# Kernel optimization log

Measured on AMD Instinct MI355X. Metric: run time of the kernel, lower is better.

## Reference

```python
import jax, jax.numpy as jnp
import numpy as np

B, S, D = 2, 2048, 1024
H = 16
HD = D // H


def setup_inputs() -> dict:
    key = jax.random.key(0)
    ks = jax.random.split(key, 6)
    x = jax.random.normal(ks[0], (B, S, D), dtype=jnp.float32)
    scale = 1.0 / np.sqrt(D)
    Wq = jax.random.normal(ks[1], (D, D), dtype=jnp.float32) * scale
    Wk = jax.random.normal(ks[2], (D, D), dtype=jnp.float32) * scale
    Wv = jax.random.normal(ks[3], (D, D), dtype=jnp.float32) * scale
    Wo = jax.random.normal(ks[4], (D, D), dtype=jnp.float32) * scale
    bo = jax.random.normal(ks[5], (D,), dtype=jnp.float32) * 0.01
    return {"x": x, "Wq": Wq, "Wk": Wk, "Wv": Wv, "Wo": Wo, "bo": bo}


def reference(x, Wq, Wk, Wv, Wo, bo):
    b, t, _ = x.shape
    # QKV projections (no bias), split into heads: [b, h, t, hd]
    q = (x @ Wq).reshape(b, t, H, HD).transpose(0, 2, 1, 3)
    k = (x @ Wk).reshape(b, t, H, HD).transpose(0, 2, 1, 3)
    v = (x @ Wv).reshape(b, t, H, HD).transpose(0, 2, 1, 3)
    # scores [b, h, t, t]; causal mask (upper triangle -> -inf) applied before scaling
    scores = jnp.einsum("bhqd,bhkd->bhqk", q, k)
    causal = jnp.triu(jnp.ones((t, t), dtype=bool), k=1)
    scores = jnp.where(causal, -jnp.inf, scores)
    attn = jax.nn.softmax(scores / jnp.sqrt(jnp.asarray(HD, scores.dtype)), axis=-1)
    ctx = jnp.einsum("bhqk,bhkd->bhqd", attn, v)
    ctx = ctx.transpose(0, 2, 1, 3).reshape(b, t, H * HD)
    return ctx @ Wo + bo
```

## Files before the change

### kernel.cpp

```cpp
#include <hip/hip_runtime.h>

#define B_ 2
#define S_ 2048
#define D_ 1024
#define H_ 16
#define HD_ 64
#define M_ (B_*S_)

typedef __attribute__((ext_vector_type(8))) short bf16x8;
typedef __attribute__((ext_vector_type(4))) short s16x4;
typedef __attribute__((ext_vector_type(4))) float f32x4;
typedef __attribute__((ext_vector_type(4))) unsigned int u32x4;

static __device__ __forceinline__ unsigned short f2bf(float f) {
  unsigned int u = __builtin_bit_cast(unsigned int, f);
  u += 0x7FFFu + ((u >> 16) & 1u);
  return (unsigned short)(u >> 16);
}

static __device__ __forceinline__ unsigned int cvt_pk_bf16(float a, float b) {
  unsigned int r;
  asm("v_cvt_pk_bf16_f32 %0, %1, %2" : "=v"(r) : "v"(a), "v"(b));
  return r;
}

static __device__ __forceinline__ void gload_lds16(const void* g, void* l) {
  __builtin_amdgcn_global_load_lds(
      (const __attribute__((address_space(1))) unsigned int*)g,
      (__attribute__((address_space(3))) unsigned int*)l, 16, 0, 0);
}

__global__ __launch_bounds__(256) void xcvt_kernel(const float* __restrict__ x,
                                                   unsigned short* __restrict__ xb) {
  size_t i = ((size_t)blockIdx.x * 256 + threadIdx.x) * 8;
  float4 a = ((const float4*)(x + i))[0];
  float4 b = ((const float4*)(x + i))[1];
  bf16x8 w;
  w[0]=(short)f2bf(a.x); w[1]=(short)f2bf(a.y); w[2]=(short)f2bf(a.z); w[3]=(short)f2bf(a.w);
  w[4]=(short)f2bf(b.x); w[5]=(short)f2bf(b.y); w[6]=(short)f2bf(b.z); w[7]=(short)f2bf(b.w);
  *(bf16x8*)(xb + i) = w;
}

__global__ void wtrans_kernel(const float* __restrict__ Wq, const float* __restrict__ Wk,
                              const float* __restrict__ Wv, const float* __restrict__ Wo,
                              unsigned short* __restrict__ wt) {
  __shared__ float tile[32][33];
  const float* W = blockIdx.z==0 ? Wq : blockIdx.z==1 ? Wk : blockIdx.z==2 ? Wv : Wo;
  unsigned short* out = wt + (size_t)blockIdx.z * D_ * D_;
  int n0 = blockIdx.x*32, k0 = blockIdx.y*32;
  int tx = threadIdx.x, ty = threadIdx.y;
  #pragma unroll
  for (int i=0;i<4;i++) tile[ty+i*8][tx] = W[(size_t)(k0+ty+i*8)*D_ + n0+tx];
  __syncthreads();
  #pragma unroll
  for (int i=0;i<4;i++) out[(size_t)(n0+ty+i*8)*D_ + (k0+tx)] = f2bf(tile[tx][ty+i*8]);
}

#define GEMM_K_LOOP(Abase, Bbase)                                                     \
  for (int ks = 0; ks < 16; ++ks) {                                                   \
    const int k0 = ks * 64;                                                           \
    __syncthreads();                                                                  \
    _Pragma("unroll")                                                                 \
    for (int p = 0; p < 4; ++p) {                                                     \
      int c = p*256 + t;                                                              \
      int row = c >> 3, sl = (c & 7) ^ (row & 7);                                     \
      gload_lds16(Abase + (size_t)row*D_ + k0 + sl*8, &As[(p*256 + wid*64)*8]);       \
    }                                                                                 \
    _Pragma("unroll")                                                                 \
    for (int p = 0; p < 4; ++p) {                                                     \
      int c = p*256 + t;                                                              \
      int row = c >> 3, sl = (c & 7) ^ (row & 7);                                     \
      gload_lds16(Bbase + (size_t)row*D_ + k0 + sl*8, &Bs[(p*256 + wid*64)*8]);       \
    }                                                                                 \
    __syncthreads();                                                                  \
    _Pragma("unroll")                                                                 \
    for (int kk = 0; kk < 2; ++kk) {                                                  \
      bf16x8 af[4], bfr[4];                                                           \
      _Pragma("unroll")                                                               \
      for (int m = 0; m < 4; ++m) {                                                   \
        int row = wr + m*16 + l15;                                                    \
        af[m] = *(const bf16x8*)((const char*)As + row*128 + (((kk*4+lg)^(row&7))<<4)); \
      }                                                                               \
      _Pragma("unroll")                                                               \
      for (int n = 0; n < 4; ++n) {                                                   \
        int row = wc + n*16 + l15;                                                    \
        bfr[n] = *(const bf16x8*)((const char*)Bs + row*128 + (((kk*4+lg)^(row&7))<<4)); \
      }                                                                               \
      _Pragma("unroll")                                                               \
      for (int m = 0; m < 4; ++m)                                                     \
        _Pragma("unroll")                                                             \
        for (int n = 0; n < 4; ++n)                                                   \
          acc[m][n] = __builtin_amdgcn_mfma_f32_16x16x32_bf16(af[m], bfr[n], acc[m][n], 0,0,0); \
    }                                                                                 \
  }

__global__ __launch_bounds__(256,3) void gemm_qkv_kernel(
    const unsigned short* __restrict__ xb, const unsigned short* __restrict__ wt,
    unsigned short* __restrict__ Qo, unsigned short* __restrict__ Ko,
    unsigned short* __restrict__ Vto) {
  __shared__ __align__(16) unsigned short As[128*64];
  __shared__ __align__(16) unsigned short Bs[128*64];
  const int z = blockIdx.z;
  const int m0 = blockIdx.y*128, n0 = blockIdx.x*128;
  const int t = threadIdx.x, lane = t & 63, wid = t >> 6;
  const int wr = (wid>>1)*64, wc = (wid&1)*64;
  const int l15 = lane & 15, lg = lane >> 4;
  const unsigned short* Ab = xb + (size_t)m0 * D_;
  const unsigned short* Bb = wt + (size_t)z * D_ * D_ + (size_t)n0 * D_;

  f32x4 acc[4][4];
  #pragma unroll
  for (int m=0;m<4;m++)
    #pragma unroll
    for (int n=0;n<4;n++) acc[m][n] = f32x4{0.f,0.f,0.f,0.f};

  GEMM_K_LOOP(Ab, Bb)

  const float qscale = 0.18033688011112042f;
  #pragma unroll
  for (int m=0;m<4;m++) {
    #pragma unroll
    for (int n=0;n<4;n++) {
      #pragma unroll
      for (int r=0;r<4;r++) {
        int gm = m0 + wr + m*16 + lg*4 + r;
        int gn = n0 + wc + n*16 + l15;
        int b = gm >> 11, s = gm & (S_-1);
        int h = gn >> 6,  d = gn & 63;
        float av = acc[m][n][r];
        if (z==0) av *= qscale;
        unsigned short val = f2bf(av);
        if (z==0)      Qo[(((size_t)(b*H_+h))*S_ + s)*HD_ + d] = val;
        else if (z==1) Ko[(((size_t)(b*H_+h))*S_ + s)*HD_ + d] = val;
        else           Vto[(((size_t)(b*H_+h))*HD_ + d)*S_ + s] = val;
      }
    }
  }
}

__global__ __launch_bounds__(256,3) void attn_kernel(
    const unsigned short* __restrict__ Q, const unsigned short* __restrict__ K,
    const unsigned short* __restrict__ Vt, unsigned short* __restrict__ ctx) {
  __shared__ __align__(16) unsigned short KT[2][64*64];
  __shared__ __align__(16) unsigned short VT[2][64*64];
  __shared__ float LS[2][64];
  const int t = threadIdx.x, lane = t & 63, wid = t >> 6;
  const int bh = blockIdx.x & 31;
  const int qt = 31 - (int)(blockIdx.x >> 5);
  const int b = bh >> 4, h = bh & 15;
  const int q0 = qt * 64;
  const int nchunk = qt + 1;
  const unsigned short* Qp = Q  + (size_t)bh * S_ * HD_;
  const unsigned short* Kp = K  + (size_t)bh * S_ * HD_;
  const unsigned short* Vp = Vt + (size_t)bh * HD_ * S_;
  const int l15 = lane & 15, lg = lane >> 4;
  const int rsub = lane >> 3, slot = lane & 7;
  const int sslot = slot ^ rsub;

  bf16x8 qf0[4], qf1[4];
  #pragma unroll
  for (int j=0;j<4;j++) {
    qf0[j] = *(const bf16x8*)(Qp + (size_t)(q0 + j*16 + l15)*HD_ + lg*8);
    qf1[j] = *(const bf16x8*)(Qp + (size_t)(q0 + j*16 + l15)*HD_ + 32 + lg*8);
  }

  f32x4 o[4][4];
  f32x4 accl[4];
  #pragma unroll
  for (int j=0;j<4;j++) {
    accl[j] = f32x4{0.f,0.f,0.f,0.f};
    #pragma unroll
    for (int dt=0;dt<4;dt++) o[j][dt] = f32x4{0.f,0.f,0.f,0.f};
  }
  s16x4 ones;
  ones[0] = (short)0x3F80; ones[1] = (short)0x3F80;
  ones[2] = (short)0x3F80; ones[3] = (short)0x3F80;

  const unsigned short* kS0 = Kp + (size_t)(16*wid + rsub)*HD_ + sslot*8;
  const unsigned short* kS1 = kS0 + 8*HD_;
  const unsigned short* vS0 = Vp + (size_t)(16*wid + rsub)*S_ + sslot*8;
  const unsigned short* vS1 = vS0 + 8*S_;

  auto stage = [&](int buf) {
    unsigned short* kd = &KT[buf][16*wid*64];
    unsigned short* vd = &VT[buf][16*wid*64];
    gload_lds16(kS0, kd);
    gload_lds16(kS1, kd + 8*64);
    gload_lds16(vS0, vd);
    gload_lds16(vS1, vd + 8*64);
    kS0 += 64*HD_; kS1 += 64*HD_;
    vS0 += 64;     vS1 += 64;
  };

  const int krow = wid*16 + l15;
  const int ksw = (krow & 7) << 4;

  auto body = [&](int cur, bool domask) {
    const char* Kt = (const char*)&KT[cur][0];
    const char* Vv = (const char*)&VT[cur][0];

    bf16x8 kf0 = *(const bf16x8*)(Kt + krow*128 + ((lg*16)      ^ ksw));
    bf16x8 kf1 = *(const bf16x8*)(Kt + krow*128 + ((64 + lg*16) ^ ksw));
    s16x4 vb[4];
    #pragma unroll
    for (int dt=0;dt<4;dt++) {
      int vrow = dt*16 + l15;
      int vsw = (vrow & 7) << 4;
      vb[dt] = *(const s16x4*)(Vv + vrow*128 + ((wid*32 + lg*8) ^ vsw));
    }

    f32x4 st[4];
    __builtin_amdgcn_s_setprio(1);
    #pragma unroll
    for (int j=0;j<4;j++) {
      f32x4 z = f32x4{0.f,0.f,0.f,0.f};
      z = __builtin_amdgcn_mfma_f32_16x16x32_bf16(kf0, qf0[j], z, 0,0,0);
      z = __builtin_amdgcn_mfma_f32_16x16x32_bf16(kf1, qf1[j], z, 0,0,0);
      st[j] = z;
    }
    __builtin_amdgcn_s_setprio(0);

    if (domask) {
      #pragma unroll
      for (int j=0;j<4;j++)
        #pragma unroll
        for (int r=0;r<4;r++)
          if (wid*16 + lg*4 + r > j*16 + l15) st[j][r] = -INFINITY;
    }

    s16x4 pa[4];
    #pragma unroll
    for (int j=0;j<4;j++) {
      float p0 = exp2f(st[j][0]);
      float p1 = exp2f(st[j][1]);
      float p2 = exp2f(st[j][2]);
      float p3 = exp2f(st[j][3]);
      uint2 u;
      u.x = cvt_pk_bf16(p0, p1);
      u.y = cvt_pk_bf16(p2, p3);
      pa[j] = __builtin_bit_cast(s16x4, u);
    }

    __builtin_amdgcn_s_setprio(1);
    #pragma unroll
    for (int j=0;j<4;j++)
      accl[j] = __builtin_amdgcn_mfma_f32_16x16x16bf16_1k(pa[j], ones, accl[j], 0,0,0);
    #pragma unroll
    for (int j=0;j<4;j++)
      #pragma unroll
      for (int dt=0;dt<4;dt++)
        o[j][dt] = __builtin_amdgcn_mfma_f32_16x16x16bf16_1k(pa[j], vb[dt], o[j][dt], 0,0,0);
    __builtin_amdgcn_s_setprio(0);
  };

  stage(0);
  __syncthreads();

  int cur = 0;
  for (int ch=0; ch<nchunk-1; ++ch) {
    stage(cur^1);
    body(cur, false);
    __syncthreads();
    cur ^= 1;
  }
  body(cur, true);

  float* bufA = (float*)&KT[0][0];
  float* bufB = (float*)&VT[0][0];
  __syncthreads();

  if (wid & 1) {
    float* dst = (wid == 1) ? bufA : bufB;
    #pragma unroll
    for (int j=0;j<4;j++) {
      #pragma unroll
      for (int dt=0;dt<4;dt++)
        #pragma unroll
        for (int r=0;r<4;r++)
          dst[(j*16 + lg*4 + r)*64 + dt*16 + l15] = o[j][dt][r];
      if (l15 == 0)
        #pragma unroll
        for (int r=0;r<4;r++) LS[wid>>1][j*16 + lg*4 + r] = accl[j][r];
    }
  }
  __syncthreads();
  if (!(wid & 1)) {
    float* src = (wid == 0) ? bufA : bufB;
    #pragma unroll
    for (int j=0;j<4;j++) {
      #pragma unroll
      for (int dt=0;dt<4;dt++)
        #pragma unroll
        for (int r=0;r<4;r++)
          o[j][dt][r] += src[(j*16 + lg*4 + r)*64 + dt*16 + l15];
      #pragma unroll
      for (int r=0;r<4;r++) accl[j][r] += LS[wid>>1][j*16 + lg*4 + r];
    }
  }
  __syncthreads();
  if (wid == 2) {
    #pragma unroll
    for (int j=0;j<4;j++) {
      #pragma unroll
      for (int dt=0;dt<4;dt++)
        #pragma unroll
        for (int r=0;r<4;r++)
          bufA[(j*16 + lg*4 + r)*64 + dt*16 + l15] = o[j][dt][r];
      if (l15 == 0)
        #pragma unroll
        for (int r=0;r<4;r++) LS[0][j*16 + lg*4 + r] = accl[j][r];
    }
  }
  __syncthreads();
  if (wid == 0) {
    #pragma unroll
    for (int j=0;j<4;j++) {
      #pragma unroll
      for (int dt=0;dt<4;dt++)
        #pragma unroll
        for (int r=0;r<4;r++)
          o[j][dt][r] += bufA[(j*16 + lg*4 + r)*64 + dt*16 + l15];
      #pragma unroll
      for (int r=0;r<4;r++) accl[j][r] += LS[0][j*16 + lg*4 + r];
      float lr[4];
      #pragma unroll
      for (int r=0;r<4;r++) lr[r] = 1.f / accl[j][r];
      #pragma unroll
      for (int dt=0;dt<4;dt++)
        #pragma unroll
        for (int r=0;r<4;r++) {
          size_t row = (size_t)(b*S_ + q0 + j*16 + lg*4 + r);
          ctx[row*D_ + h*HD_ + dt*16 + l15] = f2bf(o[j][dt][r] * lr[r]);
        }
    }
  }
}

__global__ __launch_bounds__(256,3) void gemm_out_kernel(
    const unsigned short* __restrict__ ctx, const unsigned short* __restrict__ WtO,
    const float* __restrict__ bo, float* __restrict__ out) {
  __shared__ __align__(16) unsigned short As[128*64];
  __shared__ __align__(16) unsigned short Bs[128*64];
  const int m0 = blockIdx.y*128, n0 = blockIdx.x*128;
  const int t = threadIdx.x, lane = t & 63, wid = t >> 6;
  const int wr = (wid>>1)*64, wc = (wid&1)*64;
  const int l15 = lane & 15, lg = lane >> 4;
  const unsigned short* Ab = ctx + (size_t)m0 * D_;
  const unsigned short* Bb = WtO + (size_t)n0 * D_;

  f32x4 acc[4][4];
  #pragma unroll
  for (int m=0;m<4;m++)
    #pragma unroll
    for (int n=0;n<4;n++) acc[m][n] = f32x4{0.f,0.f,0.f,0.f};

  GEMM_K_LOOP(Ab, Bb)

  #pragma unroll
  for (int n=0;n<4;n++) {
    float bias = bo[n0 + wc + n*16 + l15];
    #pragma unroll
    for (int m=0;m<4;m++)
      #pragma unroll
      for (int r=0;r<4;r++) {
        int gm = m0 + wr + m*16 + lg*4 + r;
        int gn = n0 + wc + n*16 + l15;
        out[(size_t)gm*D_ + gn] = acc[m][n][r] + bias;
      }
  }
}

extern "C" void kernel_launch(void* const* d_in, const int* in_sizes, int n_in,
                              void* d_out, int out_size, void* d_ws, size_t ws_size,
                              hipStream_t stream) {
  (void)in_sizes; (void)n_in; (void)out_size; (void)ws_size;
  const float* x  = (const float*)d_in[0];
  const float* Wq = (const float*)d_in[1];
  const float* Wk = (const float*)d_in[2];
  const float* Wv = (const float*)d_in[3];
  const float* Wo = (const float*)d_in[4];
  const float* bo = (const float*)d_in[5];
  float* out = (float*)d_out;

  unsigned short* wt  = (unsigned short*)d_ws;
  unsigned short* Qb  = wt  + (size_t)4*D_*D_;
  unsigned short* Kb  = Qb  + (size_t)M_*D_;
  unsigned short* Vtb = Kb  + (size_t)M_*D_;
  unsigned short* ctb = Vtb + (size_t)M_*D_;
  unsigned short* xbb = ctb + (size_t)M_*D_;

  xcvt_kernel<<<dim3(M_*D_/(256*8)), 256, 0, stream>>>(x, xbb);
  wtrans_kernel<<<dim3(32,32,4), dim3(32,8), 0, stream>>>(Wq, Wk, Wv, Wo, wt);
  gemm_qkv_kernel<<<dim3(8,32,3), 256, 0, stream>>>(xbb, wt, Qb, Kb, Vtb);
  attn_kernel<<<dim3(1024), 256, 0, stream>>>(Qb, Kb, Vtb, ctb);
  gemm_out_kernel<<<dim3(8,32), 256, 0, stream>>>(ctb, wt + (size_t)3*D_*D_, bo, out);
}
```

Baseline: 113.4 us.

## Give each wave private K/V LDS staging to drop per-chunk block barriers

Each wave now stages into its own private LDS region only the K rows and V columns it consumes. Synchronisation moves from block-wide __syncthreads to per-wave vmcnt/lgkmcnt waits, with a two-deep prefetch that refills a buffer right after its fragments are read into registers. The V staging layout and swizzle are redone to match, and launch bounds rise to 4 blocks per CU. Removing the block barriers lets waves run out of step, at the cost of more register pressure and hand-tuned wait counts that must match the issue order.

```diff
diff --git a/kernel.cpp b/kernel.cpp
--- a/kernel.cpp
+++ b/kernel.cpp
@@ -138,11 +138,10 @@
   }
 }
 
-__global__ __launch_bounds__(256,3) void attn_kernel(
+__global__ __launch_bounds__(256,4) void attn_kernel(
     const unsigned short* __restrict__ Q, const unsigned short* __restrict__ K,
     const unsigned short* __restrict__ Vt, unsigned short* __restrict__ ctx) {
-  __shared__ __align__(16) unsigned short KT[2][64*64];
-  __shared__ __align__(16) unsigned short VT[2][64*64];
+  __shared__ __align__(16) unsigned short SMEM[4][4096];
   __shared__ float LS[2][64];
   const int t = threadIdx.x, lane = t & 63, wid = t >> 6;
   const int bh = blockIdx.x & 31;
@@ -157,6 +156,9 @@
   const int rsub = lane >> 3, slot = lane & 7;
   const int sslot = slot ^ rsub;
 
+  unsigned short* kbase = &SMEM[wid][0];
+  unsigned short* vbase = &SMEM[wid][2048];
+
   bf16x8 qf0[4], qf1[4];
   #pragma unroll
   for (int j=0;j<4;j++) {
@@ -178,36 +180,41 @@
 
   const unsigned short* kS0 = Kp + (size_t)(16*wid + rsub)*HD_ + sslot*8;
   const unsigned short* kS1 = kS0 + 8*HD_;
-  const unsigned short* vS0 = Vp + (size_t)(16*wid + rsub)*S_ + sslot*8;
-  const unsigned short* vS1 = vS0 + 8*S_;
+  const int vrow32 = lane >> 1;
+  const int vks = (lane & 1) ^ ((lane >> 2) & 1);
+  const unsigned short* vS0 = Vp + (size_t)vrow32*S_ + 16*wid + vks*8;
+  const unsigned short* vS1 = vS0 + (size_t)32*S_;
 
   auto stage = [&](int buf) {
-    unsigned short* kd = &KT[buf][16*wid*64];
-    unsigned short* vd = &VT[buf][16*wid*64];
+    unsigned short* kd = kbase + buf*1024;
+    unsigned short* vd = vbase + buf*1024;
     gload_lds16(kS0, kd);
-    gload_lds16(kS1, kd + 8*64);
+    gload_lds16(kS1, kd + 512);
     gload_lds16(vS0, vd);
-    gload_lds16(vS1, vd + 8*64);
+    gload_lds16(vS1, vd + 512);
     kS0 += 64*HD_; kS1 += 64*HD_;
     vS0 += 64;     vS1 += 64;
   };
 
-  const int krow = wid*16 + l15;
-  const int ksw = (krow & 7) << 4;
-
-  auto body = [&](int cur, bool domask) {
-    const char* Kt = (const char*)&KT[cur][0];
-    const char* Vv = (const char*)&VT[cur][0];
-
-    bf16x8 kf0 = *(const bf16x8*)(Kt + krow*128 + ((lg*16)      ^ ksw));
-    bf16x8 kf1 = *(const bf16x8*)(Kt + krow*128 + ((64 + lg*16) ^ ksw));
+  const int ksw = (l15 & 7) << 4;
+  const int ksr = (lg >> 1) ^ ((l15 >> 1) & 1);
+
+  auto do_chunk = [&](int cur, bool domask, bool dostage) {
+    const char* Kt = (const char*)(kbase + cur*1024);
+    const char* Vv = (const char*)(vbase + cur*1024);
+
+    bf16x8 kf0 = *(const bf16x8*)(Kt + l15*128 + ((lg*16)      ^ ksw));
+    bf16x8 kf1 = *(const bf16x8*)(Kt + l15*128 + ((64 + lg*16) ^ ksw));
     s16x4 vb[4];
     #pragma unroll
     for (int dt=0;dt<4;dt++) {
-      int vrow = dt*16 + l15;
-      int vsw = (vrow & 7) << 4;
-      vb[dt] = *(const s16x4*)(Vv + vrow*128 + ((wid*32 + lg*8) ^ vsw));
-    }
+      int row32 = (dt&1)*16 + l15;
+      vb[dt] = *(const s16x4*)(Vv + (dt>>1)*1024 + row32*32 + ksr*16 + (lg&1)*8);
+    }
+
+    asm volatile("s_waitcnt lgkmcnt(0)" ::: "memory");
+    __builtin_amdgcn_sched_barrier(0);
+    if (dostage) stage(cur);
 
     f32x4 st[4];
     __builtin_amdgcn_s_setprio(1);
@@ -254,19 +261,21 @@
   };
 
   stage(0);
-  __syncthreads();
+  if (nchunk > 1) stage(1);
 
   int cur = 0;
   for (int ch=0; ch<nchunk-1; ++ch) {
-    stage(cur^1);
-    body(cur, false);
-    __syncthreads();
+    asm volatile("s_waitcnt vmcnt(4)" ::: "memory");
+    __builtin_amdgcn_sched_barrier(0);
+    do_chunk(cur, false, ch+2 < nchunk);
     cur ^= 1;
   }
-  body(cur, true);
-
-  float* bufA = (float*)&KT[0][0];
-  float* bufB = (float*)&VT[0][0];
+  asm volatile("s_waitcnt vmcnt(0)" ::: "memory");
+  __builtin_amdgcn_sched_barrier(0);
+  do_chunk(cur, true, false);
+
+  float* bufA = (float*)&SMEM[0][0];
+  float* bufB = (float*)&SMEM[2][0];
   __syncthreads();
 
   if (wid & 1) {
```

Result: slower. 177.5 us (+56.5%).
